# Kernel tuning notes

Measured on AMD Instinct MI355X. Metric: run time of the kernel, lower is better.

The kernel has to match this reference:

```python
import jax, jax.numpy as jnp
import numpy as np

S, B, H, V = 64, 8, 512, 8192  # seq_length, batch, hidden, vocab
NEG = -1e9  # finite stand-in for -inf so gradients stay clean


def setup_inputs() -> dict:
    key = jax.random.key(0)
    ks = jax.random.split(key, 8)
    lin = lambda k, fi, fo: jax.random.normal(k, (fi, fo), jnp.float32) * 0.05
    return dict(
        h=jax.random.normal(ks[0], (S, B, H), jnp.float32) * 0.1,
        sentence=jax.random.randint(ks[1], (S, B), 0, V),
        t_W1=lin(ks[2], 2 * H, H), t_b1=jnp.zeros((H,), jnp.float32),
        t_W2=lin(ks[3], H, 1), t_b2=jnp.zeros((1,), jnp.float32),
        w_W1=lin(ks[4], 2 * H, H), w_b1=jnp.zeros((H,), jnp.float32),
        w_W2=lin(ks[5], H, V), w_b2=jnp.zeros((V,), jnp.float32),
    )


def _inside(h, sentence, t_W1, t_b1, t_W2, t_b2, w_W1, w_b1, w_W2, w_b2):
    sent_length = S - 1
    # ---- transition scores on full (i, j) grid: concat(h_i, h_j) -> MLP -> scalar
    hi = jnp.broadcast_to(h[:, None], (S, S, B, H))
    hj = jnp.broadcast_to(h[None, :], (S, S, B, H))
    feat = jnp.concatenate([hi, hj], axis=-1)                      # [S,S,B,2H]
    t = (jax.nn.relu(feat @ t_W1 + t_b1) @ t_W2 + t_b2)[..., 0]    # [S,S,B]
    sh_lp = jax.nn.log_sigmoid(-t)   # log p(shift | i, j)
    re_lp = jax.nn.log_sigmoid(t)    # log p(reduce | i, j)

    # ---- word generation log-probs for pairs (i, j), i < j <= sent_length-1
    iu, ju = jnp.triu_indices(sent_length, k=1)                    # P pairs
    hp = jnp.concatenate([h[iu], h[ju]], axis=-1)                  # [P,B,2H]
    logits = jax.nn.relu(hp @ w_W1 + w_b1) @ w_W2 + w_b2           # [P,B,V]
    lse = jax.scipy.special.logsumexp(logits, axis=-1)             # [P,B]
    tok = sentence[ju + 1]                                         # [P,B]
    tok_logit = jnp.take_along_axis(logits, tok[..., None], axis=-1)[..., 0]
    word_lp = tok_logit - lse
    # shift prob + word prob (word_prob_list in the original)
    wp = jnp.full((S, S, B), NEG, jnp.float32).at[iu, ju].set(sh_lp[iu, ju] + word_lp)

    # ---- DP table init
    table = jnp.full((S, S, B), NEG, jnp.float32)
    f0 = jnp.concatenate([h[0], h[0]], axis=-1)                    # [B,2H]
    lg0 = jax.nn.relu(f0 @ w_W1 + w_b1) @ w_W2 + w_b2              # [B,V]
    init_lp = jnp.take_along_axis(jax.nn.log_softmax(lg0, axis=-1),
                                  sentence[1][:, None], axis=1)[:, 0]
    table = table.at[0, 1].set(init_lp)
    jd = jnp.arange(1, sent_length)
    table = table.at[jd, jd + 1].set(0.0)

    # ---- diagonal sweep: table[i,j] = LSE_k( table[i,k]+table[k,j]+wp[i,k]+re[k,j] )
    ivec = jnp.arange(S)
    mvec = jnp.arange(1, S)

    def step(tab, g):
        i = ivec[:, None]
        m = mvec[None, :]
        k = jnp.clip(i + m, 0, S - 1)                              # [S,S-1]
        jv = jnp.clip(ivec + g, 0, S - 1)                          # [S]
        j = jv[:, None]
        valid = (m < g) & (ivec[:, None] + g <= sent_length)       # [S,S-1]
        sc = tab[i, k] + tab[k, j] + wp[i, k] + re_lp[k, j]        # [S,S-1,B]
        sc = jnp.where(valid[..., None], sc, NEG)
        mmax = jnp.max(sc, axis=1, keepdims=True)
        new = jnp.log(jnp.sum(jnp.exp(sc - mmax), axis=1)) + mmax[:, 0]
        row_ok = (ivec + g <= sent_length)[:, None]
        tab = tab.at[ivec, jv].set(jnp.where(row_ok, new, tab[ivec, jv]))
        return tab, None

    table, _ = jax.lax.scan(step, table, jnp.arange(2, sent_length + 1))
    final = table[0, sent_length] + re_lp[0, sent_length]          # [B]
    return -jnp.sum(final)  # neg_log_likelihood


def reference(h, sentence, t_W1, t_b1, t_W2, t_b2, w_W1, w_b1, w_W2, w_b2):
    return _inside(h, sentence, t_W1, t_b1, t_W2, t_b2, w_W1, w_b1, w_W2, w_b2)
```

## Files before the change

kernel.cpp:

```cpp
#include <hip/hip_runtime.h>
#include <hip/hip_bf16.h>
#include <hip/hip_fp8.h>
#include <math.h>

#define NEG (-1.0e9f)

typedef __bf16 bf16_t;
typedef __bf16 bf16x4 __attribute__((ext_vector_type(4)));
typedef __bf16 bf16x8 __attribute__((ext_vector_type(8)));
typedef float f32x4 __attribute__((ext_vector_type(4)));
typedef unsigned char u8;

#define SS 64
#define BB 8
#define HH 512
#define VV 8192
#define NPAIR 1953
#define NPTOT 1954
#define MROWS (NPTOT*BB)
#define MPAD  16384

__device__ __forceinline__ float logsig(float x) {
  return fminf(x, 0.f) - __logf(1.f + __expf(-fabsf(x)));
}
__device__ __forceinline__ u8 f2q(float x) { __hip_fp8_e4m3 q(x); return q.__x; }
__device__ __forceinline__ float q2f(u8 b) { __hip_fp8_e4m3 q; q.__x = b; return (float)q; }

__global__ __launch_bounds__(256) void k_prep(
    const float* __restrict__ h,   bf16_t* __restrict__ hbf,
    const float* __restrict__ tW1, bf16_t* __restrict__ tW1T,
    const float* __restrict__ wW1, bf16_t* __restrict__ wW1T,
    const float* __restrict__ wW2, u8* __restrict__ w2t8) {
  __shared__ float tile[32][33];
  int blk = blockIdx.x, tid = threadIdx.x;
  if (blk < 256) {
    int gi = blk * 256 + tid;
    float4 v = ((const float4*)h)[gi];
    bf16x4 o = {(bf16_t)v.x, (bf16_t)v.y, (bf16_t)v.z, (bf16_t)v.w};
    ((bf16x4*)hbf)[gi] = o;
    return;
  }
  if (blk < 1280) {
    const float* in; bf16_t* out; int R = 1024, C = 512, t;
    if (blk < 768) { in = tW1; out = tW1T; t = blk - 256; }
    else           { in = wW1; out = wW1T; t = blk - 768; }
    int xt = C / 32;
    int c0 = (t % xt) * 32, r0 = (t / xt) * 32;
    int tx = tid & 31, ty = tid >> 5;
    for (int i = ty; i < 32; i += 8)
      tile[i][tx] = in[(size_t)(r0 + i) * C + c0 + tx];
    __syncthreads();
    for (int i = ty; i < 32; i += 8)
      out[(size_t)(c0 + i) * R + r0 + tx] = (bf16_t)tile[tx][i];
    return;
  }
  int t = blk - 1280;
  int c0 = (t % 256) * 32, r0 = (t / 256) * 32;
  int tx = tid & 31, ty = tid >> 5;
  for (int i = ty; i < 32; i += 8)
    tile[i][tx] = wW2[(size_t)(r0 + i) * 8192 + c0 + tx];
  __syncthreads();
  for (int i = ty; i < 32; i += 8)
    w2t8[(size_t)(c0 + i) * 512 + r0 + tx] = f2q(tile[tx][i]);
}

__global__ __launch_bounds__(256) void k_gemm4(
    const bf16_t* __restrict__ A,
    const bf16_t* __restrict__ tW1T, const bf16_t* __restrict__ wW1T,
    float* __restrict__ Ut, float* __restrict__ Vt,
    float* __restrict__ Uw, float* __restrict__ Vw)
{
  __shared__ __align__(16) bf16_t As[128 * 32];
  __shared__ __align__(16) bf16_t Bs[128 * 32];
  const int tid = threadIdx.x;
  const int lane = tid & 63;
  const int wave = tid >> 6;
  const int wr = wave >> 1, wc = wave & 1;
  const int sel = blockIdx.x >> 4, sub = blockIdx.x & 15;
  const bf16_t* BT = (sel < 2 ? tW1T : wW1T) + (sel & 1) * 512;
  float* Cout = (sel == 0) ? Ut : (sel == 1) ? Vt : (sel == 2) ? Uw : Vw;
  const int m0 = (sub & 3) * 128, n0 = (sub >> 2) * 128;
  const int lda = 512, ldb = 1024, ldc = 512;

  const int rowS = tid >> 2;
  const int kS = (tid & 3) * 8;
  const bf16_t* gA0 = A + (size_t)(m0 + rowS) * lda + kS;
  const bf16_t* gA1 = A + (size_t)(m0 + rowS + 64) * lda + kS;
  const bf16_t* gB0 = BT + (size_t)(n0 + rowS) * ldb + kS;
  const bf16_t* gB1 = BT + (size_t)(n0 + rowS + 64) * ldb + kS;

  f32x4 acc[4][4] = {};
  const int aoff = (wr * 64 + (lane & 15)) * 32 + (lane >> 4) * 8;
  const int boff = (wc * 64 + (lane & 15)) * 32 + (lane >> 4) * 8;

  for (int k0 = 0; k0 < 512; k0 += 32) {
    __builtin_amdgcn_global_load_lds((const __attribute__((address_space(1))) void*)(gA0 + k0),
        (__attribute__((address_space(3))) void*)(As + wave * 512), 16, 0, 0);
    __builtin_amdgcn_global_load_lds((const __attribute__((address_space(1))) void*)(gA1 + k0),
        (__attribute__((address_space(3))) void*)(As + 2048 + wave * 512), 16, 0, 0);
    __builtin_amdgcn_global_load_lds((const __attribute__((address_space(1))) void*)(gB0 + k0),
        (__attribute__((address_space(3))) void*)(Bs + wave * 512), 16, 0, 0);
    __builtin_amdgcn_global_load_lds((const __attribute__((address_space(1))) void*)(gB1 + k0),
        (__attribute__((address_space(3))) void*)(Bs + 2048 + wave * 512), 16, 0, 0);
    __syncthreads();
    bf16x8 af[4], bfr[4];
    #pragma unroll
    for (int mf = 0; mf < 4; ++mf) af[mf] = *(const bf16x8*)&As[aoff + mf * 16 * 32];
    #pragma unroll
    for (int nf = 0; nf < 4; ++nf) bfr[nf] = *(const bf16x8*)&Bs[boff + nf * 16 * 32];
    #pragma unroll
    for (int mf = 0; mf < 4; ++mf)
      #pragma unroll
      for (int nf = 0; nf < 4; ++nf)
        acc[mf][nf] = __builtin_amdgcn_mfma_f32_16x16x32_bf16(af[mf], bfr[nf], acc[mf][nf], 0, 0, 0);
    __syncthreads();
  }
  #pragma unroll
  for (int mf = 0; mf < 4; ++mf)
    #pragma unroll
    for (int r2 = 0; r2 < 4; ++r2) {
      int grow = m0 + wr * 64 + mf * 16 + (lane >> 4) * 4 + r2;
      #pragma unroll
      for (int nf = 0; nf < 4; ++nf) {
        int gcol = n0 + wc * 64 + nf * 16 + (lane & 15);
        Cout[(size_t)grow * ldc + gcol] = acc[mf][nf][r2];
      }
    }
}

#define STAGEA(b, h, kt) do { \
  const u8* _s = A8 + (size_t)(m0 + (h)*128 + (tid>>2)) * 512 + (kt)*64 + csrc; \
  __builtin_amdgcn_global_load_lds((const __attribute__((address_space(1))) void*)_s, \
    (__attribute__((address_space(3))) void*)(As + (b)*16384 + (h)*8192 + (tid>>6)*1024), 16, 0, 0); \
} while(0)

#define STAGEB(b, h, kt) do { \
  const u8* _s = BT8 + (size_t)(n0 + (h)*128 + (tid>>2)) * 512 + (kt)*64 + csrc; \
  __builtin_amdgcn_global_load_lds((const __attribute__((address_space(1))) void*)_s, \
    (__attribute__((address_space(3))) void*)(Bs + (b)*16384 + (h)*8192 + (tid>>6)*1024), 16, 0, 0); \
} while(0)

#define LDA(b, mh) do { \
  _Pragma("unroll") \
  for (int _m = 0; _m < 4; ++_m) { \
    _Pragma("unroll") \
    for (int _k = 0; _k < 2; ++_k) \
      af[_m][_k] = *(const long*)(As + (b)*16384 + (mh)*8192 + aoffs[_m][_k]); \
  } \
} while(0)

#define LDB(b, nh) do { \
  _Pragma("unroll") \
  for (int _n = 0; _n < 2; ++_n) { \
    _Pragma("unroll") \
    for (int _k = 0; _k < 2; ++_k) \
      bfr[nh][_n][_k] = *(const long*)(Bs + (b)*16384 + (nh)*8192 + boffs[_n][_k]); \
  } \
} while(0)

#define MMA(mh, nh) do { \
  __builtin_amdgcn_s_setprio(1); \
  _Pragma("unroll") \
  for (int _m = 0; _m < 4; ++_m) \
    _Pragma("unroll") \
    for (int _n = 0; _n < 2; ++_n) \
      _Pragma("unroll") \
      for (int _k = 0; _k < 2; ++_k) \
        acc[(mh)*4+_m][(nh)*2+_n] = __builtin_amdgcn_mfma_f32_16x16x32_fp8_fp8( \
            af[_m][_k], bfr[nh][_n][_k], acc[(mh)*4+_m][(nh)*2+_n], 0, 0, 0); \
  __builtin_amdgcn_s_setprio(0); \
} while(0)

#define BARLG() do { __builtin_amdgcn_s_barrier(); \
  asm volatile("s_waitcnt lgkmcnt(0)" ::: "memory"); \
  __builtin_amdgcn_sched_barrier(0); } while(0)
#define ENDPH() __builtin_amdgcn_s_barrier()
#define CKPT() asm volatile("s_waitcnt vmcnt(2)" ::: "memory")

__global__ __launch_bounds__(512, 2) void k_gemm256(
    const u8* __restrict__ A8,
    const u8* __restrict__ BT8,
    const float* __restrict__ bias,
    float* __restrict__ sumexp)
{
  __shared__ __align__(16) u8 As[2 * 16384];
  __shared__ __align__(16) u8 Bs[2 * 16384];
  const int tid = threadIdx.x;
  const int l = tid & 63;
  const int wave = tid >> 6;
  const int wr = wave >> 2, wc = wave & 3;

  const int xcd = blockIdx.x & 7, sub = blockIdx.x >> 3;
  const int mt = xcd * 8 + (sub & 7);
  const int nt = sub >> 3;
  const int m0 = mt * 256, n0 = nt * 256;

  const int csrc = (((tid & 3) ^ ((tid >> 3) & 3)) << 4);
  int aoffs[4][2], boffs[2][2];
  #pragma unroll
  for (int mf = 0; mf < 4; ++mf) {
    int row = wr * 64 + mf * 16 + (l & 15);
    int swz = (row >> 1) & 3;
    #pragma unroll
    for (int kk = 0; kk < 2; ++kk) {
      int u8i = (l >> 4) + kk * 4;
      aoffs[mf][kk] = row * 64 + (((u8i >> 1) ^ swz) << 4) + (u8i & 1) * 8;
    }
  }
  #pragma unroll
  for (int nf = 0; nf < 2; ++nf) {
    int row = wc * 32 + nf * 16 + (l & 15);
    int swz = (row >> 1) & 3;
    #pragma unroll
    for (int kk = 0; kk < 2; ++kk) {
      int u8i = (l >> 4) + kk * 4;
      boffs[nf][kk] = row * 64 + (((u8i >> 1) ^ swz) << 4) + (u8i & 1) * 8;
    }
  }

  f32x4 acc[8][4] = {};
  long af[4][2];
  long bfr[2][2][2];

  STAGEA(0, 0, 0); STAGEA(0, 1, 0); STAGEB(0, 0, 0); STAGEB(0, 1, 0);
  STAGEA(1, 0, 1); STAGEB(1, 0, 1);
  CKPT();
  __builtin_amdgcn_s_barrier();

  #pragma unroll 1
  for (int t = 0; t < 4; ++t) {
    int tA = 2 * t + 1;
    int tB = 2 * t + 2; if (tB > 7) tB = 7;
    int tC = 2 * t + 3; if (tC > 7) tC = 7;
    LDA(0, 0); LDB(0, 0); STAGEA(1, 1, tA); BARLG(); MMA(0, 0); ENDPH();
    LDB(0, 1);            STAGEB(1, 1, tA); BARLG(); MMA(0, 1); ENDPH();
    LDA(0, 1);            STAGEA(0, 0, tB); BARLG(); MMA(1, 0); ENDPH();
                          STAGEB(0, 0, tB); BARLG(); MMA(1, 1); CKPT(); ENDPH();
    LDA(1, 0); LDB(1, 0); STAGEA(0, 1, tB); BARLG(); MMA(0, 0); ENDPH();
    LDB(1, 1);            STAGEB(0, 1, tB); BARLG(); MMA(0, 1); ENDPH();
    LDA(1, 1);            STAGEA(1, 0, tC); BARLG(); MMA(1, 0); ENDPH();
                          STAGEB(1, 0, tC); BARLG(); MMA(1, 1); CKPT(); ENDPH();
  }

  float b2v[4];
  #pragma unroll
  for (int nf = 0; nf < 4; ++nf)
    b2v[nf] = bias[n0 + (nf >> 1) * 128 + wc * 32 + (nf & 1) * 16 + (l & 15)];
  #pragma unroll
  for (int mf = 0; mf < 8; ++mf) {
    #pragma unroll
    for (int r2 = 0; r2 < 4; ++r2) {
      float s = 0.f;
      #pragma unroll
      for (int nf = 0; nf < 4; ++nf)
        s += __expf(acc[mf][nf][r2] + b2v[nf]);
      s += __shfl_xor(s, 1); s += __shfl_xor(s, 2);
      s += __shfl_xor(s, 4); s += __shfl_xor(s, 8);
      if ((l & 15) == 0)
        atomicAdd(&sumexp[m0 + (mf >> 2) * 128 + wr * 64 + (mf & 3) * 16 + (l >> 4) * 4 + r2], s);
    }
  }
}

__global__ __launch_bounds__(256) void k_act(const float* __restrict__ Uw, const float* __restrict__ Vw,
                                             const float* __restrict__ b1, u8* __restrict__ act8,
                                             float* __restrict__ sumexp) {
  int p = blockIdx.x;
  if (threadIdx.x < 8) sumexp[p * 8 + threadIdx.x] = 0.f;
  int iu = 0, ju = 0;
  bool real = (p < NPTOT);
  if (p < NPAIR) {
    int i = 0, base = 0;
    while (base + (62 - i) <= p) { base += 62 - i; ++i; }
    iu = i; ju = i + 1 + (p - base);
  }
  for (int idx = threadIdx.x; idx < BB * HH; idx += 256) {
    int b = idx >> 9, c = idx & 511;
    float v = 0.f;
    if (real) {
      v = Uw[(size_t)(iu * BB + b) * HH + c] + Vw[(size_t)(ju * BB + b) * HH + c] + b1[c];
      v = fmaxf(v, 0.f);
    }
    act8[(size_t)(p * BB + b) * HH + c] = f2q(v);
  }
}

__global__ __launch_bounds__(256) void k_tnet(const float* __restrict__ Ut, const float* __restrict__ Vt,
                                              const float* __restrict__ b1, const float* __restrict__ W2,
                                              const float* __restrict__ b2,
                                              float* __restrict__ sh_lp, float* __restrict__ re_lp) {
  int gid = blockIdx.x * 4 + (threadIdx.x >> 6);
  int lane = threadIdx.x & 63;
  int b = gid & 7, j = (gid >> 3) & 63, i = gid >> 9;
  const float4* u = (const float4*)(Ut + (size_t)(i * BB + b) * HH);
  const float4* v = (const float4*)(Vt + (size_t)(j * BB + b) * HH);
  const float4* bb = (const float4*)b1;
  const float4* ww = (const float4*)W2;
  float s = 0.f;
  #pragma unroll
  for (int qq = 0; qq < 2; ++qq) {
    int c = lane * 2 + qq;
    float4 uu = u[c], vv = v[c], b4 = bb[c], w4 = ww[c];
    s += fmaxf(uu.x + vv.x + b4.x, 0.f) * w4.x;
    s += fmaxf(uu.y + vv.y + b4.y, 0.f) * w4.y;
    s += fmaxf(uu.z + vv.z + b4.z, 0.f) * w4.z;
    s += fmaxf(uu.w + vv.w + b4.w, 0.f) * w4.w;
  }
  #pragma unroll
  for (int off = 1; off < 64; off <<= 1) s += __shfl_xor(s, off);
  if (lane == 0) {
    float t = s + b2[0];
    re_lp[gid] = logsig(t);
    sh_lp[gid] = logsig(-t);
  }
}

__global__ __launch_bounds__(256) void k_toklogit(const u8* __restrict__ act8, const u8* __restrict__ w2t8,
                                                  const float* __restrict__ b2, const int* __restrict__ sent,
                                                  float* __restrict__ tok_logit) {
  int r = blockIdx.x * 4 + (threadIdx.x >> 6);
  int lane = threadIdx.x & 63;
  int p = r >> 3, b = r & 7;
  int tok;
  if (p >= NPAIR) {
    tok = sent[1 * BB + b];
  } else {
    int i = 0, base = 0;
    while (base + (62 - i) <= p) { base += 62 - i; ++i; }
    int ju = i + 1 + (p - base);
    tok = sent[(ju + 1) * BB + b];
  }
  unsigned long av = *(const unsigned long*)(act8 + (size_t)r * 512 + lane * 8);
  unsigned long wv = *(const unsigned long*)(w2t8 + (size_t)tok * 512 + lane * 8);
  float s = 0.f;
  #pragma unroll
  for (int e = 0; e < 8; ++e)
    s += q2f((u8)(av >> (8 * e))) * q2f((u8)(wv >> (8 * e)));
  #pragma unroll
  for (int off = 1; off < 64; off <<= 1) s += __shfl_xor(s, off);
  if (lane == 0) tok_logit[r] = s + b2[tok];
}

__global__ __launch_bounds__(1024) void k_dp(const float* __restrict__ sh_lp, const float* __restrict__ re_lp,
                                             const float* __restrict__ tok_logit, const float* __restrict__ sumexp,
                                             float* __restrict__ finals) {
  int b = blockIdx.x;
  __shared__ float tab[4096];
  __shared__ float wpl[4096];
  __shared__ float rel[4096];
  int tid = threadIdx.x;
  for (int idx = tid; idx < 4096; idx += 1024) {
    tab[idx] = NEG;
    int i = idx >> 6, j = idx & 63;
    float w = NEG;
    if (i < j && j <= 62) {
      int p = i * 62 - i * (i - 1) / 2 + (j - i - 1);
      int r = p * 8 + b;
      w = sh_lp[idx * 8 + b] + (tok_logit[r] - __logf(sumexp[r]));
    }
    wpl[idx] = w;
    rel[idx] = re_lp[idx * 8 + b];
  }
  __syncthreads();
  if (tid == 0) tab[1] = tok_logit[NPAIR * 8 + b] - __logf(sumexp[NPAIR * 8 + b]);
  if (tid >= 1 && tid <= 62) tab[tid * 64 + tid + 1] = 0.f;
  __syncthreads();
  int lane = tid & 63, wave = tid >> 6;
  for (int g = 2; g <= 63; ++g) {
    int cnt = 64 - g;
    if (g <= 17) {
      int seg = lane >> 4, sl = lane & 15;
      int i = wave * 4 + seg;
      if (i < cnt) {
        int m = sl + 1;
        int j = i + g, k = i + m;
        float sc = NEG;
        if (m < g) sc = tab[i * 64 + k] + tab[k * 64 + j] + wpl[i * 64 + k] + rel[k * 64 + j];
        float mx = sc;
        #pragma unroll
        for (int off = 1; off < 16; off <<= 1) mx = fmaxf(mx, __shfl_xor(mx, off));
        float e = (m < g) ? __expf(sc - mx) : 0.f;
        #pragma unroll
        for (int off = 1; off < 16; off <<= 1) e += __shfl_xor(e, off);
        if (sl == 0) tab[i * 64 + j] = __logf(e) + mx;
      }
    } else {
      for (int i = wave; i < cnt; i += 16) {
        int m = lane + 1;
        int j = i + g, k = i + m;
        float sc = NEG;
        if (m < g) sc = tab[i * 64 + k] + tab[k * 64 + j] + wpl[i * 64 + k] + rel[k * 64 + j];
        float mx = sc;
        #pragma unroll
        for (int off = 1; off < 64; off <<= 1) mx = fmaxf(mx, __shfl_xor(mx, off));
        float e = (m < g) ? __expf(sc - mx) : 0.f;
        #pragma unroll
        for (int off = 1; off < 64; off <<= 1) e += __shfl_xor(e, off);
        if (lane == 0) tab[i * 64 + j] = __logf(e) + mx;
      }
    }
    __syncthreads();
  }
  if (tid == 0) finals[b] = tab[63] + rel[63];
}

__global__ void k_final(const float* __restrict__ finals, float* __restrict__ out) {
  if (threadIdx.x == 0) {
    float s = 0.f;
    for (int b = 0; b < 8; ++b) s += finals[b];
    out[0] = -s;
  }
}

extern "C" void kernel_launch(void* const* d_in, const int* in_sizes, int n_in,
                              void* d_out, int out_size, void* d_ws, size_t ws_size,
                              hipStream_t stream) {
  const float* h    = (const float*)d_in[0];
  const int*   sent = (const int*)d_in[1];
  const float* tW1  = (const float*)d_in[2];
  const float* tb1  = (const float*)d_in[3];
  const float* tW2  = (const float*)d_in[4];
  const float* tb2  = (const float*)d_in[5];
  const float* wW1  = (const float*)d_in[6];
  const float* wb1  = (const float*)d_in[7];
  const float* wW2  = (const float*)d_in[8];
  const float* wb2  = (const float*)d_in[9];
  float* out = (float*)d_out;

  char* ws = (char*)d_ws;
  size_t off = 0;
  auto alloc = [&](size_t bytes) { char* p = ws + off; off += (bytes + 255) & ~(size_t)255; return p; };
  bf16_t* hbf    = (bf16_t*)alloc((size_t)512 * 512 * 2);
  bf16_t* tW1T   = (bf16_t*)alloc((size_t)512 * 1024 * 2);
  bf16_t* wW1T   = (bf16_t*)alloc((size_t)512 * 1024 * 2);
  u8*     w2t8   = (u8*)alloc((size_t)VV * HH);
  float*  Ut     = (float*)alloc((size_t)512 * 512 * 4);
  float*  Vt     = (float*)alloc((size_t)512 * 512 * 4);
  float*  Uw     = (float*)alloc((size_t)512 * 512 * 4);
  float*  Vw     = (float*)alloc((size_t)512 * 512 * 4);
  u8*     act8   = (u8*)alloc((size_t)MPAD * HH);
  float*  sumexp = (float*)alloc((size_t)MPAD * 4);
  float*  tokl   = (float*)alloc((size_t)MPAD * 4);
  float*  shlp   = (float*)alloc((size_t)32768 * 4);
  float*  relp   = (float*)alloc((size_t)32768 * 4);
  float*  finals = (float*)alloc(256);

  k_prep<<<5376, 256, 0, stream>>>(h, hbf, tW1, tW1T, wW1, wW1T, wW2, w2t8);
  k_gemm4<<<64, 256, 0, stream>>>(hbf, tW1T, wW1T, Ut, Vt, Uw, Vw);
  k_act<<<MPAD / 8, 256, 0, stream>>>(Uw, Vw, wb1, act8, sumexp);
  k_tnet<<<32768 / 4, 256, 0, stream>>>(Ut, Vt, tb1, tW2, tb2, shlp, relp);
  k_gemm256<<<2048, 512, 0, stream>>>(act8, w2t8, wb2, sumexp);
  k_toklogit<<<MROWS / 4, 256, 0, stream>>>(act8, w2t8, wb2, sent, tokl);
  k_dp<<<8, 1024, 0, stream>>>(shlp, relp, tokl, sumexp, finals);
  k_final<<<1, 64, 0, stream>>>(finals, out);
}
```

Baseline: 320.3 us.

## Permute fp8 K-layout so GEMM fragments load as 16-byte LDS reads

Stores activations and the transposed W2 weights in a permuted K order within each 64-byte chunk, so each lane's two 8-byte MFMA K-fragments become adjacent. The big GEMM's LDS reads then become single 16-byte vector loads instead of pairs of 8-byte loads, which cuts LDS instruction count and address arithmetic. The activation kernel is also vectorized to read float4 and write packed 8-byte fp8 groups. The permutation has to match on both operands and across the swizzle; the dot product in the token-logit kernel still holds because both sides use the same layout.

```diff
diff --git a/kernel.cpp b/kernel.cpp
--- a/kernel.cpp
+++ b/kernel.cpp
@@ -9,7 +9,9 @@
 typedef __bf16 bf16x4 __attribute__((ext_vector_type(4)));
 typedef __bf16 bf16x8 __attribute__((ext_vector_type(8)));
 typedef float f32x4 __attribute__((ext_vector_type(4)));
+typedef long i64x2 __attribute__((ext_vector_type(2)));
 typedef unsigned char u8;
+typedef unsigned long long u64;
 
 #define SS 64
 #define BB 8
@@ -25,6 +27,7 @@
 }
 __device__ __forceinline__ u8 f2q(float x) { __hip_fp8_e4m3 q(x); return q.__x; }
 __device__ __forceinline__ float q2f(u8 b) { __hip_fp8_e4m3 q; q.__x = b; return (float)q; }
+__device__ __forceinline__ int ksl(int c) { return 2 * (c & 3) + (c >> 2); }
 
 __global__ __launch_bounds__(256) void k_prep(
     const float* __restrict__ h,   bf16_t* __restrict__ hbf,
@@ -60,8 +63,11 @@
   for (int i = ty; i < 32; i += 8)
     tile[i][tx] = wW2[(size_t)(r0 + i) * 8192 + c0 + tx];
   __syncthreads();
-  for (int i = ty; i < 32; i += 8)
-    w2t8[(size_t)(c0 + i) * 512 + r0 + tx] = f2q(tile[tx][i]);
+  for (int i = ty; i < 32; i += 8) {
+    int k = r0 + tx;
+    int pos = (k >> 6) * 64 + ksl((k >> 3) & 7) * 8 + (k & 7);
+    w2t8[(size_t)(c0 + i) * 512 + pos] = f2q(tile[tx][i]);
+  }
 }
 
 __global__ __launch_bounds__(256) void k_gemm4(
@@ -142,20 +148,14 @@
 
 #define LDA(b, mh) do { \
   _Pragma("unroll") \
-  for (int _m = 0; _m < 4; ++_m) { \
-    _Pragma("unroll") \
-    for (int _k = 0; _k < 2; ++_k) \
-      af[_m][_k] = *(const long*)(As + (b)*16384 + (mh)*8192 + aoffs[_m][_k]); \
-  } \
+  for (int _m = 0; _m < 4; ++_m) \
+    afv[_m] = *(const i64x2*)(As + (b)*16384 + (mh)*8192 + ardE + _m*1024); \
 } while(0)
 
 #define LDB(b, nh) do { \
   _Pragma("unroll") \
-  for (int _n = 0; _n < 2; ++_n) { \
-    _Pragma("unroll") \
-    for (int _k = 0; _k < 2; ++_k) \
-      bfr[nh][_n][_k] = *(const long*)(Bs + (b)*16384 + (nh)*8192 + boffs[_n][_k]); \
-  } \
+  for (int _n = 0; _n < 2; ++_n) \
+    bfv[nh][_n] = *(const i64x2*)(Bs + (b)*16384 + (nh)*8192 + brdE + _n*1024); \
 } while(0)
 
 #define MMA(mh, nh) do { \
@@ -163,11 +163,12 @@
   _Pragma("unroll") \
   for (int _m = 0; _m < 4; ++_m) \
     _Pragma("unroll") \
-    for (int _n = 0; _n < 2; ++_n) \
-      _Pragma("unroll") \
-      for (int _k = 0; _k < 2; ++_k) \
-        acc[(mh)*4+_m][(nh)*2+_n] = __builtin_amdgcn_mfma_f32_16x16x32_fp8_fp8( \
-            af[_m][_k], bfr[nh][_n][_k], acc[(mh)*4+_m][(nh)*2+_n], 0, 0, 0); \
+    for (int _n = 0; _n < 2; ++_n) { \
+      acc[(mh)*4+_m][(nh)*2+_n] = __builtin_amdgcn_mfma_f32_16x16x32_fp8_fp8( \
+          afv[_m][0], bfv[nh][_n][0], acc[(mh)*4+_m][(nh)*2+_n], 0, 0, 0); \
+      acc[(mh)*4+_m][(nh)*2+_n] = __builtin_amdgcn_mfma_f32_16x16x32_fp8_fp8( \
+          afv[_m][1], bfv[nh][_n][1], acc[(mh)*4+_m][(nh)*2+_n], 0, 0, 0); \
+    } \
   __builtin_amdgcn_s_setprio(0); \
 } while(0)
 
@@ -196,31 +197,13 @@
   const int m0 = mt * 256, n0 = nt * 256;
 
   const int csrc = (((tid & 3) ^ ((tid >> 3) & 3)) << 4);
-  int aoffs[4][2], boffs[2][2];
-  #pragma unroll
-  for (int mf = 0; mf < 4; ++mf) {
-    int row = wr * 64 + mf * 16 + (l & 15);
-    int swz = (row >> 1) & 3;
-    #pragma unroll
-    for (int kk = 0; kk < 2; ++kk) {
-      int u8i = (l >> 4) + kk * 4;
-      aoffs[mf][kk] = row * 64 + (((u8i >> 1) ^ swz) << 4) + (u8i & 1) * 8;
-    }
-  }
-  #pragma unroll
-  for (int nf = 0; nf < 2; ++nf) {
-    int row = wc * 32 + nf * 16 + (l & 15);
-    int swz = (row >> 1) & 3;
-    #pragma unroll
-    for (int kk = 0; kk < 2; ++kk) {
-      int u8i = (l >> 4) + kk * 4;
-      boffs[nf][kk] = row * 64 + (((u8i >> 1) ^ swz) << 4) + (u8i & 1) * 8;
-    }
-  }
+  const int rsw = (((l >> 4) ^ ((l & 15) >> 1)) & 3) << 4;
+  const int ardE = (wr * 64 + (l & 15)) * 64 + rsw;
+  const int brdE = (wc * 32 + (l & 15)) * 64 + rsw;
 
   f32x4 acc[8][4] = {};
-  long af[4][2];
-  long bfr[2][2][2];
+  i64x2 afv[4];
+  i64x2 bfv[2][2];
 
   STAGEA(0, 0, 0); STAGEA(0, 1, 0); STAGEB(0, 0, 0); STAGEB(0, 1, 0);
   STAGEA(1, 0, 1); STAGEB(1, 0, 1);
@@ -274,14 +257,23 @@
     while (base + (62 - i) <= p) { base += 62 - i; ++i; }
     iu = i; ju = i + 1 + (p - base);
   }
-  for (int idx = threadIdx.x; idx < BB * HH; idx += 256) {
-    int b = idx >> 9, c = idx & 511;
-    float v = 0.f;
+  for (int t = threadIdx.x; t < 512; t += 256) {
+    int b = t >> 6, c = t & 63;
+    u64 bytes = 0;
     if (real) {
-      v = Uw[(size_t)(iu * BB + b) * HH + c] + Vw[(size_t)(ju * BB + b) * HH + c] + b1[c];
-      v = fmaxf(v, 0.f);
+      const float4* u4 = (const float4*)(Uw + (size_t)(iu * BB + b) * HH);
+      const float4* v4 = (const float4*)(Vw + (size_t)(ju * BB + b) * HH);
+      const float4* bb4 = (const float4*)b1;
+      #pragma unroll
+      for (int q = 0; q < 2; ++q) {
+        float4 uu = u4[c * 2 + q], vv = v4[c * 2 + q], bb = bb4[c * 2 + q];
+        bytes |= (u64)f2q(fmaxf(uu.x + vv.x + bb.x, 0.f)) << (8 * (q * 4 + 0));
+        bytes |= (u64)f2q(fmaxf(uu.y + vv.y + bb.y, 0.f)) << (8 * (q * 4 + 1));
+        bytes |= (u64)f2q(fmaxf(uu.z + vv.z + bb.z, 0.f)) << (8 * (q * 4 + 2));
+        bytes |= (u64)f2q(fmaxf(uu.w + vv.w + bb.w, 0.f)) << (8 * (q * 4 + 3));
+      }
     }
-    act8[(size_t)(p * BB + b) * HH + c] = f2q(v);
+    *(u64*)(act8 + (size_t)(p * 8 + b) * 512 + (c >> 3) * 64 + ksl(c & 7) * 8) = bytes;
   }
 }
 
@@ -330,8 +322,8 @@
     int ju = i + 1 + (p - base);
     tok = sent[(ju + 1) * BB + b];
   }
-  unsigned long av = *(const unsigned long*)(act8 + (size_t)r * 512 + lane * 8);
-  unsigned long wv = *(const unsigned long*)(w2t8 + (size_t)tok * 512 + lane * 8);
+  u64 av = *(const u64*)(act8 + (size_t)r * 512 + lane * 8);
+  u64 wv = *(const u64*)(w2t8 + (size_t)tok * 512 + lane * 8);
   float s = 0.f;
   #pragma unroll
   for (int e = 0; e < 8; ++e)
```

Result: faster. 297.5 us (-7.1%).
